# Optimization experiments

Hardware: AMD Instinct MI355X
Metric: run time of the kernel (lower is better)

The kernel has to match this reference:

```python
import jax, jax.numpy as jnp
import numpy as np

HIDDEN = 2048
HEADS = 16
HEAD_DIM = HIDDEN // HEADS


def setup_inputs() -> dict:
    key = jax.random.key(0)
    kx, kq, kk, kv, ko = jax.random.split(key, 5)
    s = 1.0 / np.sqrt(HIDDEN)
    return {
        "x": jax.random.normal(kx, (2, 2048, HIDDEN), dtype=jnp.float32),
        "Wq": jax.random.normal(kq, (HIDDEN, HIDDEN), dtype=jnp.float32) * s,
        "Wk": jax.random.normal(kk, (HIDDEN, HIDDEN), dtype=jnp.float32) * s,
        "Wv": jax.random.normal(kv, (HIDDEN, HIDDEN), dtype=jnp.float32) * s,
        "Wo": jax.random.normal(ko, (HIDDEN, HIDDEN), dtype=jnp.float32) * s,
    }


def reference(x, Wq, Wk, Wv, Wo):
    B, S, H = x.shape
    nh, hd = HEADS, HEAD_DIM
    # projections (nn.Linear: y = x @ W.T; here W stored as [in, out] so x @ W)
    q = (x @ Wq).reshape(B, S, nh, hd).transpose(0, 2, 1, 3)  # [B,nh,S,hd]
    k = (x @ Wk).reshape(B, S, nh, hd).transpose(0, 2, 1, 3)
    v = (x @ Wv).reshape(B, S, nh, hd).transpose(0, 2, 1, 3)
    scores = jnp.einsum("bhqd,bhkd->bhqk", q, k) / jnp.sqrt(jnp.float32(hd))
    causal = jnp.tril(jnp.ones((S, S), dtype=bool))  # keep lower triangle
    scores = jnp.where(causal, scores, jnp.finfo(scores.dtype).min)
    attn = jax.nn.softmax(scores, axis=-1)
    out = jnp.einsum("bhqk,bhkd->bhqd", attn, v)
    out = out.transpose(0, 2, 1, 3).reshape(B, S, H)
    return out @ Wo
```

## Files before the change

### kernel.cpp

```cpp
#include <hip/hip_runtime.h>
#include <stdint.h>

typedef unsigned short u16;
typedef __bf16 bf16x8 __attribute__((ext_vector_type(8)));
typedef float f32x4 __attribute__((ext_vector_type(4)));

#define B_ 2
#define S_ 2048
#define H_ 2048
#define NH_ 16
#define HD_ 128

__device__ __forceinline__ u16 f2bf(float f) {
    uint32_t u = __float_as_uint(f);
    u += 0x7fff + ((u >> 16) & 1);
    return (u16)(u >> 16);
}

__device__ __forceinline__ void gl_lds16(const u16* g, u16* l) {
    __builtin_amdgcn_global_load_lds(
        (const __attribute__((address_space(1))) void*)g,
        (__attribute__((address_space(3))) void*)l, 16, 0, 0);
}

__global__ __launch_bounds__(256) void cast_x_kernel(const float* __restrict__ x, u16* __restrict__ xb) {
    int i = (blockIdx.x * 256 + threadIdx.x) * 4;
    float4 v = *(const float4*)&x[i];
    ushort4 o;
    o.x = f2bf(v.x); o.y = f2bf(v.y); o.z = f2bf(v.z); o.w = f2bf(v.w);
    *(ushort4*)&xb[i] = o;
}

__global__ __launch_bounds__(256) void transpose_cast_kernel(
        const float* __restrict__ w0, const float* __restrict__ w1,
        const float* __restrict__ w2, const float* __restrict__ w3,
        u16* __restrict__ dqkv, u16* __restrict__ dwo) {
    int z = blockIdx.z;
    const float* src = (z == 0) ? w0 : (z == 1) ? w1 : (z == 2) ? w2 : w3;
    u16* dst = (z < 3) ? (dqkv + (size_t)z * H_ * H_) : dwo;
    __shared__ float tile[32][33];
    int n0 = blockIdx.x * 32, k0 = blockIdx.y * 32;
    int tx = threadIdx.x, ty = threadIdx.y;
#pragma unroll
    for (int i = 0; i < 4; i++)
        tile[ty + i * 8][tx] = src[(size_t)(k0 + ty + i * 8) * H_ + n0 + tx];
    __syncthreads();
#pragma unroll
    for (int i = 0; i < 4; i++)
        dst[(size_t)(n0 + ty + i * 8) * H_ + k0 + tx] = f2bf(tile[tx][ty + i * 8]);
}

__global__ __launch_bounds__(256) void vtrans_kernel(const u16* __restrict__ V, u16* __restrict__ VT) {
    __shared__ u16 t[64 * 72];
    int bh = blockIdx.z;
    int s0 = blockIdx.x * 64, d0 = blockIdx.y * 64;
    const u16* src = V + (size_t)bh * S_ * HD_;
    u16* dst = VT + (size_t)bh * S_ * HD_;
    int tid = threadIdx.x;
#pragma unroll
    for (int i = 0; i < 2; i++) {
        int p = i * 256 + tid, r = p >> 3, c = p & 7;
        *(int4*)&t[r * 72 + c * 8] = *(const int4*)&src[(size_t)(s0 + r) * HD_ + d0 + c * 8];
    }
    __syncthreads();
#pragma unroll
    for (int i = 0; i < 2; i++) {
        int p = i * 256 + tid, rd = p >> 3, c = p & 7;
        u16 tmp[8];
#pragma unroll
        for (int j = 0; j < 8; j++) tmp[j] = t[(c * 8 + j) * 72 + rd];
        *(int4*)&dst[(size_t)(d0 + rd) * S_ + s0 + c * 8] = *(int4*)tmp;
    }
}

template <int MODE>
__global__ __launch_bounds__(256, 2) void gemm_bt(
        const u16* __restrict__ A, const u16* __restrict__ Bt, float* __restrict__ Cout,
        u16* __restrict__ q, u16* __restrict__ k, u16* __restrict__ v,
        int M, int N, int K) {
    __shared__ u16 As[128 * 64];
    __shared__ u16 Bs[128 * 64];
    int tid = threadIdx.x;
    int w = tid >> 6, lane = tid & 63, quad = lane >> 4, l16 = lane & 15;
    int wm = w >> 1, wn = w & 1;
    int m0 = blockIdx.y * 128, n0 = blockIdx.x * 128;

    f32x4 acc[4][4];
#pragma unroll
    for (int mi = 0; mi < 4; mi++)
#pragma unroll
        for (int ni = 0; ni < 4; ni++)
            acc[mi][ni] = (f32x4){0.f, 0.f, 0.f, 0.f};

    for (int k0 = 0; k0 < K; k0 += 64) {
        const u16* ga = A + (size_t)m0 * K + k0;
        const u16* gb = Bt + (size_t)n0 * K + k0;
#pragma unroll
        for (int j = 0; j < 4; j++) {
            int base = (j * 4 + w) * 64;
            int p = base + lane;
            int row = p >> 3;
            int c = (p & 7) ^ (row & 7);
            gl_lds16(&ga[(size_t)row * K + c * 8], &As[base * 8]);
            gl_lds16(&gb[(size_t)row * K + c * 8], &Bs[base * 8]);
        }
        __syncthreads();
#pragma unroll
        for (int ks = 0; ks < 2; ks++) {
            bf16x8 af[4], bf[4];
#pragma unroll
            for (int mi = 0; mi < 4; mi++) {
                int row = wm * 64 + mi * 16 + l16;
                af[mi] = *(const bf16x8*)&As[row * 64 + (((ks * 4 + quad) ^ (row & 7)) * 8)];
            }
#pragma unroll
            for (int ni = 0; ni < 4; ni++) {
                int row = wn * 64 + ni * 16 + l16;
                bf[ni] = *(const bf16x8*)&Bs[row * 64 + (((ks * 4 + quad) ^ (row & 7)) * 8)];
            }
#pragma unroll
            for (int mi = 0; mi < 4; mi++)
#pragma unroll
                for (int ni = 0; ni < 4; ni++)
                    acc[mi][ni] = __builtin_amdgcn_mfma_f32_16x16x32_bf16(af[mi], bf[ni], acc[mi][ni], 0, 0, 0);
        }
        __syncthreads();
    }

#pragma unroll
    for (int mi = 0; mi < 4; mi++) {
#pragma unroll
        for (int ni = 0; ni < 4; ni++) {
            int ng = n0 + wn * 64 + ni * 16 + l16;
#pragma unroll
            for (int r = 0; r < 4; r++) {
                int mg = m0 + wm * 64 + mi * 16 + quad * 4 + r;
                float val = acc[mi][ni][r];
                if (MODE == 0) {
                    int which = ng >> 11;
                    int rem = ng & 2047;
                    int h = rem >> 7, d = rem & 127;
                    int b = mg >> 11, s = mg & 2047;
                    u16* base = (which == 0) ? q : (which == 1) ? k : v;
                    base[((size_t)((b * NH_ + h) * S_ + s)) * HD_ + d] = f2bf(val);
                } else {
                    Cout[(size_t)mg * N + ng] = val;
                }
            }
        }
    }
}

__global__ __launch_bounds__(256, 2) void flash_kernel(
        const u16* __restrict__ Q, const u16* __restrict__ Kb,
        const u16* __restrict__ VT, u16* __restrict__ Ctx) {
    __shared__ u16 Ks[2][64 * 128];
    __shared__ u16 Vs[128 * 64];
    __shared__ u16 Ps[64 * 64];
    int tid = threadIdx.x;
    int w = tid >> 6, lane = tid & 63, quad = lane >> 4, l16 = lane & 15;

    int id = blockIdx.x;
    int bh = id & 31;
    int b = bh >> 4, h = bh & 15;
    int pair = id >> 5;
    int qts = pair, qtl = 31 - pair;
    int n0 = qts + 1;

    size_t bhoff = ((size_t)b * NH_ + h) * S_ * HD_;
    const u16* Qp = Q + bhoff;
    const u16* Kp = Kb + bhoff;
    const u16* Vp = VT + bhoff;

    auto stageK = [&](int t, int buf) {
        int kv0 = ((t >= n0) ? (t - n0) : t) * 64;
#pragma unroll
        for (int j = 0; j < 4; j++) {
            int base = (j * 4 + w) * 64;
            int p = base + lane;
            int row = p >> 4;
            int c = (p & 15) ^ (row & 15);
            gl_lds16(&Kp[(size_t)(kv0 + row) * HD_ + c * 8], &Ks[buf][base * 8]);
        }
    };
    auto stageV = [&](int t) {
        int kv0 = ((t >= n0) ? (t - n0) : t) * 64;
#pragma unroll
        for (int j = 0; j < 4; j++) {
            int base = (j * 4 + w) * 64;
            int p = base + lane;
            int row = p >> 3;
            int c = (p & 7) ^ (row & 7);
            gl_lds16(&Vp[(size_t)row * S_ + kv0 + c * 8], &Vs[base * 8]);
        }
    };

    int q0 = qts * 64, qw = q0 + w * 16;
    bf16x8 qf[4];
#pragma unroll
    for (int ks = 0; ks < 4; ks++)
        qf[ks] = *(const bf16x8*)&Qp[(size_t)(qw + l16) * HD_ + ks * 32 + quad * 8];

    float l_part[4] = {0.f, 0.f, 0.f, 0.f};
    f32x4 ao[8];
#pragma unroll
    for (int dt = 0; dt < 8; dt++) ao[dt] = (f32x4){0.f, 0.f, 0.f, 0.f};

    const float sl2 = 0.08838834764831845f * 1.4426950408889634f;

    auto epilogue = [&]() {
#pragma unroll
        for (int r = 0; r < 4; r++) {
            float l = l_part[r];
            l += __shfl_xor(l, 1);
            l += __shfl_xor(l, 2);
            l += __shfl_xor(l, 4);
            l += __shfl_xor(l, 8);
            float inv = 1.0f / l;
            int qg = qw + quad * 4 + r;
            size_t rowbase = ((size_t)b * S_ + qg) * H_ + h * HD_;
#pragma unroll
            for (int dt = 0; dt < 8; dt++)
                Ctx[rowbase + dt * 16 + l16] = f2bf(ao[dt][r] * inv);
        }
    };

    stageK(0, 0);

    for (int t = 0; t < 33; t++) {
        __syncthreads();
        if (t + 1 < 33) stageK(t + 1, (t + 1) & 1);
        stageV(t);
        if (t == n0) {
            epilogue();
            q0 = qtl * 64; qw = q0 + w * 16;
#pragma unroll
            for (int ks = 0; ks < 4; ks++)
                qf[ks] = *(const bf16x8*)&Qp[(size_t)(qw + l16) * HD_ + ks * 32 + quad * 8];
#pragma unroll
            for (int r = 0; r < 4; r++) l_part[r] = 0.f;
#pragma unroll
            for (int dt = 0; dt < 8; dt++) ao[dt] = (f32x4){0.f, 0.f, 0.f, 0.f};
        }
        int kv0 = ((t >= n0) ? (t - n0) : t) * 64;
        bool diag = (kv0 == q0);
        int buf = t & 1;

        f32x4 sc[4];
#pragma unroll
        for (int nt = 0; nt < 4; nt++) {
            sc[nt] = (f32x4){0.f, 0.f, 0.f, 0.f};
            int row = nt * 16 + l16;
#pragma unroll
            for (int ks = 0; ks < 4; ks++) {
                bf16x8 kf = *(const bf16x8*)&Ks[buf][row * 128 + (((ks * 4 + quad) ^ (row & 15)) * 8)];
                sc[nt] = __builtin_amdgcn_mfma_f32_16x16x32_bf16(qf[ks], kf, sc[nt], 0, 0, 0);
            }
        }

#pragma unroll
        for (int r = 0; r < 4; r++) {
            int prow = w * 16 + quad * 4 + r;
            int qg = qw + quad * 4 + r;
            float psum = 0.f;
#pragma unroll
            for (int nt = 0; nt < 4; nt++) {
                float p = exp2f(sc[nt][r] * sl2);
                if (diag && (kv0 + nt * 16 + l16 > qg)) p = 0.f;
                sc[nt][r] = p;
                psum += p;
            }
            l_part[r] += psum;
#pragma unroll
            for (int nt = 0; nt < 4; nt++) {
                int col = nt * 16 + l16;
                Ps[prow * 64 + (((col >> 3) ^ (prow & 7)) * 8) + (col & 7)] = f2bf(sc[nt][r]);
            }
        }

        __syncthreads();

#pragma unroll
        for (int kstep = 0; kstep < 2; kstep++) {
            int prow = w * 16 + l16;
            bf16x8 pf = *(const bf16x8*)&Ps[prow * 64 + (((kstep * 4 + quad) ^ (prow & 7)) * 8)];
#pragma unroll
            for (int dt = 0; dt < 8; dt++) {
                int d = dt * 16 + l16;
                bf16x8 vf = *(const bf16x8*)&Vs[d * 64 + (((kstep * 4 + quad) ^ (d & 7)) * 8)];
                ao[dt] = __builtin_amdgcn_mfma_f32_16x16x32_bf16(pf, vf, ao[dt], 0, 0, 0);
            }
        }
    }
    epilogue();
}

extern "C" void kernel_launch(void* const* d_in, const int* in_sizes, int n_in,
                              void* d_out, int out_size, void* d_ws, size_t ws_size,
                              hipStream_t stream) {
    const float* x  = (const float*)d_in[0];
    const float* Wq = (const float*)d_in[1];
    const float* Wk = (const float*)d_in[2];
    const float* Wv = (const float*)d_in[3];
    const float* Wo = (const float*)d_in[4];
    float* out = (float*)d_out;

    const size_t MB = 1024 * 1024;
    char* ws = (char*)d_ws;
    u16* Xb    = (u16*)(ws);
    u16* WqkvT = (u16*)(ws + 16 * MB);
    u16* WoT   = (u16*)(ws + 40 * MB);
    u16* Qb    = (u16*)(ws + 48 * MB);
    u16* Kbuf  = (u16*)(ws + 64 * MB);
    u16* Vbuf  = (u16*)(ws + 80 * MB);
    u16* Ctx   = (u16*)(ws + 96 * MB);
    u16* VT    = Xb;

    cast_x_kernel<<<8192, 256, 0, stream>>>(x, Xb);
    transpose_cast_kernel<<<dim3(64, 64, 4), dim3(32, 8), 0, stream>>>(Wq, Wk, Wv, Wo, WqkvT, WoT);
    gemm_bt<0><<<dim3(48, 32), 256, 0, stream>>>(Xb, WqkvT, nullptr, Qb, Kbuf, Vbuf, 4096, 6144, 2048);
    vtrans_kernel<<<dim3(32, 2, 32), 256, 0, stream>>>(Vbuf, VT);
    flash_kernel<<<512, 256, 0, stream>>>(Qb, Kbuf, VT, Ctx);
    gemm_bt<1><<<dim3(16, 32), 256, 0, stream>>>(Ctx, WoT, out, nullptr, nullptr, nullptr, 4096, 2048, 2048);
}
```

Baseline: 343.9 us.

## Compute V transposed via swapped GEMM, fold softmax scale into Q, specialize diagonal masking

The V projection is now a separate GEMM computing Wv^T·X^T, so it writes V already transposed into the layout the attention kernel reads, and the standalone V transpose kernel is removed. The softmax scale is folded into Q at the projection epilogue, which drops a multiply per score element. The attention loop gets a mask-free fast path for off-diagonal tiles, with the diagonal tile detected from the loop index. Risks: an extra GEMM launch with strided transposed stores, and Q is rounded to bf16 after scaling, which changes rounding slightly.

Measured after the change: 349.2 us. About the same (+1.5%).

```diff
diff --git a/kernel.cpp b/kernel.cpp
--- a/kernel.cpp
+++ b/kernel.cpp
@@ -10,6 +10,8 @@
 #define H_ 2048
 #define NH_ 16
 #define HD_ 128
+
+#define SL2f (0.08838834764831845f * 1.4426950408889634f)
 
 __device__ __forceinline__ u16 f2bf(float f) {
     uint32_t u = __float_as_uint(f);
@@ -34,10 +36,10 @@
 __global__ __launch_bounds__(256) void transpose_cast_kernel(
         const float* __restrict__ w0, const float* __restrict__ w1,
         const float* __restrict__ w2, const float* __restrict__ w3,
-        u16* __restrict__ dqkv, u16* __restrict__ dwo) {
+        u16* __restrict__ dqk, u16* __restrict__ dwv, u16* __restrict__ dwo) {
     int z = blockIdx.z;
     const float* src = (z == 0) ? w0 : (z == 1) ? w1 : (z == 2) ? w2 : w3;
-    u16* dst = (z < 3) ? (dqkv + (size_t)z * H_ * H_) : dwo;
+    u16* dst = (z < 2) ? (dqk + (size_t)z * H_ * H_) : ((z == 2) ? dwv : dwo);
     __shared__ float tile[32][33];
     int n0 = blockIdx.x * 32, k0 = blockIdx.y * 32;
     int tx = threadIdx.x, ty = threadIdx.y;
@@ -48,29 +50,6 @@
 #pragma unroll
     for (int i = 0; i < 4; i++)
         dst[(size_t)(n0 + ty + i * 8) * H_ + k0 + tx] = f2bf(tile[tx][ty + i * 8]);
-}
-
-__global__ __launch_bounds__(256) void vtrans_kernel(const u16* __restrict__ V, u16* __restrict__ VT) {
-    __shared__ u16 t[64 * 72];
-    int bh = blockIdx.z;
-    int s0 = blockIdx.x * 64, d0 = blockIdx.y * 64;
-    const u16* src = V + (size_t)bh * S_ * HD_;
-    u16* dst = VT + (size_t)bh * S_ * HD_;
-    int tid = threadIdx.x;
-#pragma unroll
-    for (int i = 0; i < 2; i++) {
-        int p = i * 256 + tid, r = p >> 3, c = p & 7;
-        *(int4*)&t[r * 72 + c * 8] = *(const int4*)&src[(size_t)(s0 + r) * HD_ + d0 + c * 8];
-    }
-    __syncthreads();
-#pragma unroll
-    for (int i = 0; i < 2; i++) {
-        int p = i * 256 + tid, rd = p >> 3, c = p & 7;
-        u16 tmp[8];
-#pragma unroll
-        for (int j = 0; j < 8; j++) tmp[j] = t[(c * 8 + j) * 72 + rd];
-        *(int4*)&dst[(size_t)(d0 + rd) * S_ + s0 + c * 8] = *(int4*)tmp;
-    }
 }
 
 template <int MODE>
@@ -141,8 +120,14 @@
                     int rem = ng & 2047;
                     int h = rem >> 7, d = rem & 127;
                     int b = mg >> 11, s = mg & 2047;
-                    u16* base = (which == 0) ? q : (which == 1) ? k : v;
-                    base[((size_t)((b * NH_ + h) * S_ + s)) * HD_ + d] = f2bf(val);
+                    if (which == 0)
+                        q[((size_t)((b * NH_ + h) * S_ + s)) * HD_ + d] = f2bf(val * SL2f);
+                    else
+                        k[((size_t)((b * NH_ + h) * S_ + s)) * HD_ + d] = f2bf(val);
+                } else if (MODE == 2) {
+                    int h = mg >> 7, d = mg & 127;
+                    int b = ng >> 11, s = ng & 2047;
+                    v[((size_t)((b * NH_ + h) * HD_ + d)) * S_ + s] = f2bf(val);
                 } else {
                     Cout[(size_t)mg * N + ng] = val;
                 }
@@ -205,8 +190,6 @@
     f32x4 ao[8];
 #pragma unroll
     for (int dt = 0; dt < 8; dt++) ao[dt] = (f32x4){0.f, 0.f, 0.f, 0.f};
-
-    const float sl2 = 0.08838834764831845f * 1.4426950408889634f;
 
     auto epilogue = [&]() {
 #pragma unroll
@@ -243,7 +226,7 @@
             for (int dt = 0; dt < 8; dt++) ao[dt] = (f32x4){0.f, 0.f, 0.f, 0.f};
         }
         int kv0 = ((t >= n0) ? (t - n0) : t) * 64;
-        bool diag = (kv0 == q0);
+        bool diag = (t == n0 - 1) || (t == 32);
         int buf = t & 1;
 
         f32x4 sc[4];
@@ -258,23 +241,42 @@
             }
         }
 
-#pragma unroll
-        for (int r = 0; r < 4; r++) {
-            int prow = w * 16 + quad * 4 + r;
-            int qg = qw + quad * 4 + r;
-            float psum = 0.f;
-#pragma unroll
-            for (int nt = 0; nt < 4; nt++) {
-                float p = exp2f(sc[nt][r] * sl2);
-                if (diag && (kv0 + nt * 16 + l16 > qg)) p = 0.f;
-                sc[nt][r] = p;
-                psum += p;
-            }
-            l_part[r] += psum;
-#pragma unroll
-            for (int nt = 0; nt < 4; nt++) {
-                int col = nt * 16 + l16;
-                Ps[prow * 64 + (((col >> 3) ^ (prow & 7)) * 8) + (col & 7)] = f2bf(sc[nt][r]);
+        if (!diag) {
+#pragma unroll
+            for (int r = 0; r < 4; r++) {
+                int prow = w * 16 + quad * 4 + r;
+                float psum = 0.f;
+#pragma unroll
+                for (int nt = 0; nt < 4; nt++) {
+                    float p = exp2f(sc[nt][r]);
+                    sc[nt][r] = p;
+                    psum += p;
+                }
+                l_part[r] += psum;
+#pragma unroll
+                for (int nt = 0; nt < 4; nt++) {
+                    int col = nt * 16 + l16;
+                    Ps[prow * 64 + (((col >> 3) ^ (prow & 7)) * 8) + (col & 7)] = f2bf(sc[nt][r]);
+                }
+            }
+        } else {
+#pragma unroll
+            for (int r = 0; r < 4; r++) {
+                int prow = w * 16 + quad * 4 + r;
+                int qg = qw + quad * 4 + r;
+                float psum = 0.f;
+#pragma unroll
+                for (int nt = 0; nt < 4; nt++) {
+                    float p = (kv0 + nt * 16 + l16 > qg) ? 0.f : exp2f(sc[nt][r]);
+                    sc[nt][r] = p;
+                    psum += p;
+                }
+                l_part[r] += psum;
+#pragma unroll
+                for (int nt = 0; nt < 4; nt++) {
+                    int col = nt * 16 + l16;
+                    Ps[prow * 64 + (((col >> 3) ^ (prow & 7)) * 8) + (col & 7)] = f2bf(sc[nt][r]);
+                }
             }
         }
 
@@ -307,19 +309,19 @@
 
     const size_t MB = 1024 * 1024;
     char* ws = (char*)d_ws;
-    u16* Xb    = (u16*)(ws);
-    u16* WqkvT = (u16*)(ws + 16 * MB);
-    u16* WoT   = (u16*)(ws + 40 * MB);
-    u16* Qb    = (u16*)(ws + 48 * MB);
-    u16* Kbuf  = (u16*)(ws + 64 * MB);
-    u16* Vbuf  = (u16*)(ws + 80 * MB);
-    u16* Ctx   = (u16*)(ws + 96 * MB);
-    u16* VT    = Xb;
+    u16* Xb   = (u16*)(ws);
+    u16* WqkT = (u16*)(ws + 16 * MB);
+    u16* WvT  = (u16*)(ws + 32 * MB);
+    u16* WoT  = (u16*)(ws + 40 * MB);
+    u16* Qb   = (u16*)(ws + 48 * MB);
+    u16* Kbuf = (u16*)(ws + 64 * MB);
+    u16* VT   = (u16*)(ws + 80 * MB);
+    u16* Ctx  = (u16*)(ws + 96 * MB);
 
     cast_x_kernel<<<8192, 256, 0, stream>>>(x, Xb);
-    transpose_cast_kernel<<<dim3(64, 64, 4), dim3(32, 8), 0, stream>>>(Wq, Wk, Wv, Wo, WqkvT, WoT);
-    gemm_bt<0><<<dim3(48, 32), 256, 0, stream>>>(Xb, WqkvT, nullptr, Qb, Kbuf, Vbuf, 4096, 6144, 2048);
-    vtrans_kernel<<<dim3(32, 2, 32), 256, 0, stream>>>(Vbuf, VT);
+    transpose_cast_kernel<<<dim3(64, 64, 4), dim3(32, 8), 0, stream>>>(Wq, Wk, Wv, Wo, WqkT, WvT, WoT);
+    gemm_bt<0><<<dim3(32, 32), 256, 0, stream>>>(Xb, WqkT, nullptr, Qb, Kbuf, nullptr, 4096, 4096, 2048);
+    gemm_bt<2><<<dim3(32, 16), 256, 0, stream>>>(WvT, Xb, nullptr, nullptr, nullptr, VT, 2048, 4096, 2048);
     flash_kernel<<<512, 256, 0, stream>>>(Qb, Kbuf, VT, Ctx);
     gemm_bt<1><<<dim3(16, 32), 256, 0, stream>>>(Ctx, WoT, out, nullptr, nullptr, nullptr, 4096, 2048, 2048);
 }
```
